# Performance work log

Hardware: AMD Instinct MI355X
Metric: run time of the kernel (lower is better)

## Reference

```python
import jax, jax.numpy as jnp
import numpy as np

G, N, F, H, E = 3, 40000, 256, 128, 640000


def gcn_conv(x, W, b, edge_index):
    """PyG GCNConv: x @ W, add self-loops, sym-normalized scatter-add, + bias."""
    n = x.shape[0]
    x = x @ W
    loop = jnp.arange(n)
    row = jnp.concatenate([edge_index[0], loop])  # source nodes
    col = jnp.concatenate([edge_index[1], loop])  # target nodes
    deg = jax.ops.segment_sum(jnp.ones_like(row, dtype=x.dtype), col, num_segments=n)
    dinv = jnp.where(deg > 0, jax.lax.rsqrt(jnp.maximum(deg, 1e-12)), 0.0)
    norm = dinv[row] * dinv[col]
    out = jax.ops.segment_sum(x[row] * norm[:, None], col, num_segments=n)
    return out + b


def setup_inputs() -> dict:
    key = jax.random.key(0)
    ks = jax.random.split(key, 14)
    inp = {
        'x': jax.random.normal(ks[0], (G, N, F), jnp.float32),
        'edge_index': jax.random.randint(ks[1], (G, 2, E), 0, N, jnp.int64),
        'fc1_W': jax.random.normal(ks[2], (G, F, H), jnp.float32) * 0.05,
        'fc1_b': jax.random.normal(ks[3], (G, H), jnp.float32) * 0.05,
        'conv1_W': jax.random.normal(ks[4], (G, H, H), jnp.float32) * 0.05,
        'conv1_b': jax.random.normal(ks[5], (G, H), jnp.float32) * 0.05,
        'conv2_W': jax.random.normal(ks[6], (G, H, H), jnp.float32) * 0.05,
        'conv2_b': jax.random.normal(ks[7], (G, H), jnp.float32) * 0.05,
        'dconv1_W': jax.random.normal(ks[8], (G, H, H), jnp.float32) * 0.05,
        'dconv1_b': jax.random.normal(ks[9], (G, H), jnp.float32) * 0.05,
        'dconv2_W': jax.random.normal(ks[10], (G, H, H), jnp.float32) * 0.05,
        'dconv2_b': jax.random.normal(ks[11], (G, H), jnp.float32) * 0.05,
        'fc2_W': jax.random.normal(ks[12], (H, F), jnp.float32) * 0.05,
        'fc2_b': jax.random.normal(ks[13], (F,), jnp.float32) * 0.05,
    }
    return inp


def reference(x, edge_index, fc1_W, fc1_b, conv1_W, conv1_b, conv2_W, conv2_b,
              dconv1_W, dconv1_b, dconv2_W, dconv2_b, fc2_W, fc2_b):
    def encoder(xi, ei, fw, fb, c1w, c1b, c2w, c2b):
        pre = xi @ fw + fb                     # fc1
        h = gcn_conv(pre, c1w, c1b, ei)
        h = gcn_conv(h, c2w, c2b, ei)
        return pre, jax.nn.relu(h)

    pre_feat, enc = jax.vmap(encoder)(x, edge_index, fc1_W, fc1_b,
                                      conv1_W, conv1_b, conv2_W, conv2_b)

    # Faithful reproduction of the sequentially-mutating cross-graph block.
    h = [enc[i] for i in range(G)]
    for i in range(G):
        for j in range(G):
            if j != i:
                h[i] = h[i] + h[j]
        h[i] = h[G - 1] - h[i]  # loop var j ends at G-1 (zeroes tensor when i==G-1)
        h[i] = gcn_conv(h[i], dconv1_W[i], dconv1_b[i], edge_index[i])
        h[i] = gcn_conv(h[i], dconv2_W[i], dconv2_b[i], edge_index[i])

    fin_feat = h[0]
    for k in range(1, G - 1):
        fin_feat = fin_feat + h[k]

    loss_embedding = jax.nn.softmax(fin_feat @ fc2_W + fc2_b, axis=-1)
    return pre_feat, enc, jnp.stack(h), fin_feat, loss_embedding
```

## Files before the change

kernel.cpp:

```cpp
#include <hip/hip_runtime.h>
#include <hip/hip_bf16.h>

#define NV 40000
#define FD 256
#define HD 128
#define ED 640000
#define NG 3
#define NH (NV*HD)

#define CH  64
#define EPC (ED/CH)
#define NB  625

typedef unsigned short u16;
typedef unsigned int   u32;
typedef __attribute__((ext_vector_type(8))) u16    u16x8;
typedef __attribute__((ext_vector_type(8))) __bf16 bf16x8;
typedef __attribute__((ext_vector_type(4))) float  f32x4;

__device__ inline u16 f2b(float f){ __bf16 h = (__bf16)f; return __builtin_bit_cast(u16, h); }
__device__ inline float b2f(u16 u){ u32 x = ((u32)u)<<16; return __builtin_bit_cast(float, x); }

__global__ __launch_bounds__(256) void histB_k(const int* __restrict__ ei, int* __restrict__ btot){
  int ch=blockIdx.x, g=blockIdx.y, t=threadIdx.x;
  __shared__ int h[NB];
  for (int i=t;i<NB;i+=256) h[i]=0;
  __syncthreads();
  const int* cc = ei + (long)g*2*ED + ED + ch*EPC;
  for (int j=t;j<EPC;j+=256) atomicAdd(&h[cc[j]>>6],1);
  __syncthreads();
  for (int b=t;b<NB;b+=256){ int v=h[b]; if(v) atomicAdd(&btot[g*NB+b], v); }
}

__global__ void scanB_k(const int* __restrict__ btot, int* __restrict__ base, int* __restrict__ gcur){
  __shared__ int wsum[16];
  int tid=threadIdx.x, lane=tid&63, wv=tid>>6;
  for (int g=0; g<NG; ++g){
    int v = (tid<NB)? btot[g*NB+tid] : 0;
    int s=v;
    #pragma unroll
    for (int d=1; d<64; d<<=1){ int u=__shfl_up(s,d,64); if(lane>=d) s+=u; }
    if (lane==63) wsum[wv]=s;
    __syncthreads();
    if (wv==0){
      int t3=(lane<16)?wsum[lane]:0;
      #pragma unroll
      for (int d=1; d<16; d<<=1){ int u=__shfl_up(t3,d,64); if(lane>=d) t3+=u; }
      if (lane<16) wsum[lane]=t3;
    }
    __syncthreads();
    int incl = s + (wv>0? wsum[wv-1]:0);
    if (tid<NB){
      base[g*(NB+1)+tid]=incl-v;
      gcur[g*NB+tid]=incl-v;
      if (tid==NB-1) base[g*(NB+1)+NB]=incl;
    }
    __syncthreads();
  }
}

__global__ __launch_bounds__(256) void scat_k(const int* __restrict__ ei, int* __restrict__ gcur,
                                              u32* __restrict__ temp){
  int ch=blockIdx.x, g=blockIdx.y, t=threadIdx.x;
  __shared__ int h[NB];
  __shared__ int cur[NB];
  for (int i=t;i<NB;i+=256) h[i]=0;
  __syncthreads();
  const int* rr = ei + (long)g*2*ED + ch*EPC;
  const int* cc = rr + ED;
  for (int j=t;j<EPC;j+=256) atomicAdd(&h[cc[j]>>6],1);
  __syncthreads();
  for (int b=t;b<NB;b+=256){ int v=h[b]; cur[b] = v? atomicAdd(&gcur[g*NB+b], v) : 0; }
  __syncthreads();
  u32* tg = temp + (long)g*ED;
  for (int j=t;j<EPC;j+=256){
    int r=rr[j], c=cc[j];
    int pos=atomicAdd(&cur[c>>6],1);
    tg[pos]=((u32)(c&63)<<16)|(u32)r;
  }
}

__global__ __launch_bounds__(256) void sort_k(const u32* __restrict__ temp, const int* __restrict__ base,
                                              u16* __restrict__ csr, int* __restrict__ cptr,
                                              float* __restrict__ dinv){
  int b=blockIdx.x, g=blockIdx.y, t=threadIdx.x;
  __shared__ int cnt[64];
  __shared__ int cur[64];
  if (t<64) cnt[t]=0;
  __syncthreads();
  const u32* tg = temp + (long)g*ED;
  int s=base[g*(NB+1)+b], e=base[g*(NB+1)+b+1];
  for (int i=s+t;i<e;i+=256) atomicAdd(&cnt[tg[i]>>16],1);
  __syncthreads();
  if (t<64){
    int v=cnt[t];
    int sc=v;
    #pragma unroll
    for (int d=1;d<64;d<<=1){ int u=__shfl_up(sc,d,64); if(t>=d) sc+=u; }
    int st = s + sc - v;
    cur[t]=st;
    cptr[(long)g*(NV+1) + b*64 + t] = st;
    if (b==NB-1 && t==63) cptr[(long)g*(NV+1)+NV] = e;
    dinv[(long)g*NV + b*64 + t] = rsqrtf((float)v+1.0f);
  }
  __syncthreads();
  u16* cg = csr + (long)g*ED;
  for (int i=s+t;i<e;i+=256){
    u32 tt=tg[i];
    int pos=atomicAdd(&cur[tt>>16],1);
    cg[pos]=(u16)(tt&0xFFFF);
  }
}

__global__ __launch_bounds__(256) void svec_k(const u16* __restrict__ csr, const int* __restrict__ cptr,
                                              const float* __restrict__ dinv, float* __restrict__ sv,
                                              int totWaves){
  int wid=(int)((blockIdx.x*256+threadIdx.x)>>6);
  if (wid>=totWaves) return;
  int lane=threadIdx.x&63;
  int g=wid/NV, c=wid-g*NV;
  const u16* cg=csr+(long)g*ED;
  const int* cp=cptr+(long)g*(NV+1);
  const float* dv=dinv+(long)g*NV;
  int j0=cp[c], j1=cp[c+1];
  float sum=0.f;
  for (int j=j0+lane;j<j1;j+=64) sum+=dv[cg[j]];
  #pragma unroll
  for (int o=32;o;o>>=1) sum+=__shfl_xor(sum,o,64);
  if (lane==0){ float dc=dv[c]; sv[(long)g*NV+c]=dc*(dc+sum); }
}

__device__ inline void tr_seg(const float* __restrict__ src, u16* __restrict__ dst,
                              int K, int NN, long idx, long total){
  if (idx>=total) return;
  long per=(long)K*NN; long mat=idx/per; long rem=idx-mat*per;
  int k=(int)(rem/NN), c=(int)(rem-(long)k*NN);
  dst[mat*per+(long)c*K+k]=f2b(src[idx]);
}

__global__ __launch_bounds__(256) void trall_k(
    const float* fc1W, const float* fc2W,
    const float* c1W, const float* c2W, const float* c1b,
    const float* d1W, const float* d2W, const float* d1b,
    u16* w_fc1, u16* w_fc2, u16* w_ce, u16* w_cd,
    float* t_enc, float* t_dec)
{
  int blk=blockIdx.x, t=threadIdx.x;
  if (blk < 384){
    tr_seg(fc1W, w_fc1, FD, HD, (long)blk*256+t, (long)NG*FD*HD);
  } else if (blk < 512){
    tr_seg(fc2W, w_fc2, HD, FD, (long)(blk-384)*256+t, (long)HD*FD);
  } else if (blk < 832){
    int bb=blk-512;
    int mat=bb>>6;
    int local=(bb&63)*256+t;
    int n=local>>7, k=local&127;
    const float* W1; const float* W2; u16* dst;
    if (mat<3){ W1=c1W+(long)mat*HD*HD; W2=c2W+(long)mat*HD*HD; dst=w_ce+(long)mat*HD*HD; }
    else { int md=mat-3; W1=d1W+(long)md*HD*HD; W2=d2W+(long)md*HD*HD; dst=w_cd+(long)md*HD*HD; }
    float s=0.f;
    for (int j=0;j<HD;j++) s += W1[k*HD+j]*W2[j*HD+n];
    dst[(long)n*HD+k]=f2b(s);
  } else {
    for (int idx=t; idx<768; idx+=256){
      int which=idx>>7, n=idx&127;
      const float* b; const float* W; float* dst;
      if (which<3){ b=c1b+which*HD; W=c2W+(long)which*HD*HD; dst=t_enc+which*HD; }
      else { int w2=which-3; b=d1b+w2*HD; W=d2W+(long)w2*HD*HD; dst=t_dec+w2*HD; }
      float s=0.f;
      for (int k=0;k<HD;k++) s += b[k]*W[(long)k*HD+n];
      dst[n]=s;
    }
  }
}

template<int MODE, int EX>
__global__ __launch_bounds__(256) void gemm_k(
    const void* __restrict__ A_, long sA,
    const u16* __restrict__ Bt, long sB,
    const float* __restrict__ biasCol, long sBias,
    const float* __restrict__ svec, long sS,
    const float* __restrict__ tvec,
    const float* __restrict__ scaleRow, long sSc,
    const float* __restrict__ Add,
    float* __restrict__ Cf, long sCf,
    float* __restrict__ Cf2,
    u16* __restrict__ Cb, long sCb,
    int M, int N, int K, int relu)
{
  __shared__ __align__(16) u16 lsA[128*64];
  __shared__ __align__(16) u16 lsB[128*64];
  const int gz = blockIdx.z;
  const float* Af = (const float*)A_ + (long)gz*sA;
  const u16*   Ab = (const u16*)  A_ + (long)gz*sA;
  const u16* Bp = Bt + (long)gz*sB;
  const int t = threadIdx.x;
  const int lane = t & 63, wv = t >> 6, wm = wv >> 1, wn = wv & 1;
  const int lr = lane & 15, lq = lane >> 4;
  const int ar = t >> 1, ah = t & 1;
  const long grow = (long)blockIdx.x*128 + ar;
  const int colB = blockIdx.y*128 + ar;

  f32x4 acc[4][4];
  #pragma unroll
  for (int m=0;m<4;m++)
    #pragma unroll
    for (int n=0;n<4;n++) acc[m][n] = (f32x4)(0.0f);

  for (int k0=0; k0<K; k0+=64){
    if (k0) __syncthreads();
    u16x8 av[4];
    if (grow < M){
      if (MODE==0){
        const u16x8* s = (const u16x8*)(Ab + grow*(long)K + k0 + ah*32);
        #pragma unroll
        for (int i=0;i<4;i++) av[i] = s[i];
      } else {
        const float4* s = (const float4*)(Af + grow*(long)K + k0 + ah*32);
        #pragma unroll
        for (int i=0;i<4;i++){
          float4 v0 = s[i*2], v1 = s[i*2+1];
          u16x8 w;
          w[0]=f2b(v0.x); w[1]=f2b(v0.y); w[2]=f2b(v0.z); w[3]=f2b(v0.w);
          w[4]=f2b(v1.x); w[5]=f2b(v1.y); w[6]=f2b(v1.z); w[7]=f2b(v1.w);
          av[i] = w;
        }
      }
    } else {
      #pragma unroll
      for (int i=0;i<4;i++) av[i] = (u16x8)((u16)0);
    }
    #pragma unroll
    for (int i=0;i<4;i++){
      int q = ah*4 + i;
      *(u16x8*)&lsA[ar*64 + ((q ^ (ar&7))<<3)] = av[i];
    }
    {
      const u16x8* s = (const u16x8*)(Bp + (long)colB*K + k0 + ah*32);
      #pragma unroll
      for (int i=0;i<4;i++){
        int q = ah*4 + i;
        *(u16x8*)&lsB[ar*64 + ((q ^ (ar&7))<<3)] = s[i];
      }
    }
    __syncthreads();
    #pragma unroll
    for (int kk=0; kk<2; kk++){
      bf16x8 afr[4], bfr[4];
      #pragma unroll
      for (int m=0;m<4;m++){
        int r = wm*64 + m*16 + lr;
        int q = kk*4 + lq;
        afr[m] = __builtin_bit_cast(bf16x8, *(const u16x8*)&lsA[r*64 + ((q ^ (r&7))<<3)]);
      }
      #pragma unroll
      for (int n=0;n<4;n++){
        int r = wn*64 + n*16 + lr;
        int q = kk*4 + lq;
        bfr[n] = __builtin_bit_cast(bf16x8, *(const u16x8*)&lsB[r*64 + ((q ^ (r&7))<<3)]);
      }
      #pragma unroll
      for (int m=0;m<4;m++)
        #pragma unroll
        for (int n=0;n<4;n++)
          acc[m][n] = __builtin_amdgcn_mfma_f32_16x16x32_bf16(afr[m], bfr[n], acc[m][n], 0, 0, 0);
    }
  }
  #pragma unroll
  for (int m=0;m<4;m++){
    long gr0 = (long)blockIdx.x*128 + wm*64 + m*16 + lq*4;
    #pragma unroll
    for (int n=0;n<4;n++){
      int gc = blockIdx.y*128 + wn*64 + n*16 + lr;
      float bb = biasCol[gz*sBias + gc];
      float tv = (svec!=nullptr) ? tvec[gz*sBias + gc] : 0.0f;
      #pragma unroll
      for (int i=0;i<4;i++){
        long gr = gr0 + i;
        if (gr < M){
          float v = acc[m][n][i] + bb;
          if (svec!=nullptr) v += svec[gz*sS + gr]*tv;
          if (relu) v = fmaxf(v, 0.0f);
          if (EX==0){
            if (Cf) Cf[gz*sCf + gr*(long)N + gc] = v;
            if (Cb){
              float sc = scaleRow ? scaleRow[gz*sSc + gr] : 1.0f;
              Cb[gz*sCb + gr*(long)N + gc] = f2b(v*sc);
            }
          } else if (EX==1){
            Cf[gz*sCf + gr*(long)N + gc] = v;
            float z = -(v + Add[gr*(long)N + gc]) * scaleRow[gr];
            Cb[gz*sCb + gr*(long)N + gc] = f2b(z);
          } else {
            Cf[gz*sCf + gr*(long)N + gc] = v;
            Cf2[gr*(long)N + gc] = v + Add[gr*(long)N + gc];
          }
        }
      }
    }
  }
}

__global__ __launch_bounds__(256) void agg_k(
    const u16* __restrict__ xw, long sXW,
    const u16* __restrict__ csr, long sCsr,
    const int* __restrict__ cptr, long sCp,
    const float* __restrict__ dinv, long sD,
    u16* __restrict__ outB, long sOB,
    int totWaves, int scOut)
{
  int wid = (int)((blockIdx.x*256 + threadIdx.x) >> 6);
  if (wid >= totWaves) return;
  int lane = threadIdx.x & 63;
  int g = wid / NV;
  int c = wid - g*NV;
  const u32* xp = (const u32*)(xw + (long)g*sXW);
  const u16* cg = csr + (long)g*sCsr;
  const int* cp = cptr + (long)g*sCp;
  float dc = dinv[(long)g*sD + c];
  u32 u = xp[(long)c*64 + lane];
  float sx = b2f((u16)u), sy = b2f((u16)(u>>16));
  int j0 = cp[c], j1 = cp[c+1];
  int deg = j1 - j0;
  int idx = 0;
  if (lane < deg) idx = cg[j0 + lane];
  int kmax = min(deg, 64);
  int k = 0;
  for (; k+4<=kmax; k+=4){
    int r0=__shfl(idx,k,64), r1=__shfl(idx,k+1,64), r2=__shfl(idx,k+2,64), r3=__shfl(idx,k+3,64);
    u32 v0=xp[(long)r0*64+lane], v1=xp[(long)r1*64+lane];
    u32 v2=xp[(long)r2*64+lane], v3=xp[(long)r3*64+lane];
    sx += b2f((u16)v0); sy += b2f((u16)(v0>>16));
    sx += b2f((u16)v1); sy += b2f((u16)(v1>>16));
    sx += b2f((u16)v2); sy += b2f((u16)(v2>>16));
    sx += b2f((u16)v3); sy += b2f((u16)(v3>>16));
  }
  for (; k<kmax; ++k){
    int r=__shfl(idx,k,64);
    u32 v=xp[(long)r*64+lane];
    sx += b2f((u16)v); sy += b2f((u16)(v>>16));
  }
  for (int j=j0+64; j<j1; ++j){
    int r=cg[j];
    u32 v=xp[(long)r*64+lane];
    sx += b2f((u16)v); sy += b2f((u16)(v>>16));
  }
  float m = scOut ? dc*dc : dc;
  float ox = m*sx, oy = m*sy;
  ((u32*)(outB + (long)g*sOB))[(long)c*64 + lane] = (u32)f2b(ox) | ((u32)f2b(oy)<<16);
}

__global__ void ewz_k(const float4* __restrict__ e0, const float4* __restrict__ e1,
                      const float* __restrict__ dinv0, u16* __restrict__ outB){
  int i = blockIdx.x*256 + threadIdx.x;
  if (i >= NH/4) return;
  int row = i>>5;
  float d = dinv0[row];
  float4 a = e0[i], b = e1[i];
  float x0=-d*(a.x+b.x), x1=-d*(a.y+b.y), x2=-d*(a.z+b.z), x3=-d*(a.w+b.w);
  ((uint2*)outB)[i] = make_uint2((u32)f2b(x0) | ((u32)f2b(x1)<<16),
                                 (u32)f2b(x2) | ((u32)f2b(x3)<<16));
}

__global__ void h2_k(const float* __restrict__ sv2, const float* __restrict__ t2,
                     const float* __restrict__ b2, float4* __restrict__ outF){
  int i = blockIdx.x*256 + threadIdx.x;
  if (i >= NH/4) return;
  int row = i>>5, c4 = i&31;
  float s = sv2[row];
  float4 tv = ((const float4*)t2)[c4];
  float4 bb = ((const float4*)b2)[c4];
  outF[i] = make_float4(s*tv.x+bb.x, s*tv.y+bb.y, s*tv.z+bb.z, s*tv.w+bb.w);
}

__global__ void softmax_k(float* __restrict__ d, int rows){
  int wid = (blockIdx.x*256 + threadIdx.x) >> 6;
  if (wid >= rows) return;
  int lane = threadIdx.x & 63;
  float4* p = (float4*)(d + (long)wid*FD);
  float4 v = p[lane];
  float m = fmaxf(fmaxf(v.x, v.y), fmaxf(v.z, v.w));
  #pragma unroll
  for (int o=32; o; o>>=1) m = fmaxf(m, __shfl_xor(m, o, 64));
  float e0 = __expf(v.x-m), e1 = __expf(v.y-m), e2 = __expf(v.z-m), e3 = __expf(v.w-m);
  float s = e0+e1+e2+e3;
  #pragma unroll
  for (int o=32; o; o>>=1) s += __shfl_xor(s, o, 64);
  float inv = 1.0f/s;
  p[lane] = make_float4(e0*inv, e1*inv, e2*inv, e3*inv);
}

extern "C" void kernel_launch(void* const* d_in, const int* in_sizes, int n_in,
                              void* d_out, int out_size, void* d_ws, size_t ws_size,
                              hipStream_t stream)
{
  const float* x    = (const float*)d_in[0];
  const int*   ei   = (const int*)  d_in[1];
  const float* fc1W = (const float*)d_in[2];
  const float* fc1b = (const float*)d_in[3];
  const float* c1W  = (const float*)d_in[4];
  const float* c1b  = (const float*)d_in[5];
  const float* c2W  = (const float*)d_in[6];
  const float* c2b  = (const float*)d_in[7];
  const float* d1W  = (const float*)d_in[8];
  const float* d1b  = (const float*)d_in[9];
  const float* d2W  = (const float*)d_in[10];
  const float* d2b  = (const float*)d_in[11];
  const float* fc2W = (const float*)d_in[12];
  const float* fc2b = (const float*)d_in[13];
  (void)in_sizes; (void)n_in; (void)out_size; (void)ws_size;

  float* out  = (float*)d_out;
  float* O_pre = out;
  float* O_enc = out + (long)NG*NH;
  float* O_h   = out + 2L*NG*NH;
  float* O_fin = out + 3L*NG*NH;
  float* O_ls  = O_fin + NH;

  char* p = (char*)d_ws;
  auto alloc = [&](size_t bytes)->void*{
    void* r = (void*)p; p += (bytes + 255) & ~(size_t)255; return r;
  };
  u16* bfA    = (u16*)alloc((size_t)NG*NH*2);
  u16* bfB    = (u16*)alloc((size_t)NG*NH*2);
  u16* bfC    = (u16*)alloc((size_t)NG*NH*2);
  u16* wt_fc1 = (u16*)alloc((size_t)NG*FD*HD*2);
  u16* wt_fc2 = (u16*)alloc((size_t)HD*FD*2);
  u16* wt_ce  = (u16*)alloc((size_t)NG*HD*HD*2);
  u16* wt_cd  = (u16*)alloc((size_t)2*HD*HD*2);
  float* t_enc = (float*)alloc((size_t)NG*HD*4);
  float* t_dec = (float*)alloc((size_t)NG*HD*4);
  u32*  temp  = (u32*) alloc((size_t)NG*ED*4);
  u16*  csr   = (u16*) alloc((size_t)NG*ED*2);
  int*  cptr  = (int*) alloc((size_t)NG*(NV+1)*4);
  int*  btot  = (int*) alloc((size_t)NG*NB*4);
  int*  base  = (int*) alloc((size_t)NG*(NB+1)*4);
  int*  gcur  = (int*) alloc((size_t)NG*NB*4);
  float* dinv = (float*)alloc((size_t)NG*NV*4);
  float* svec = (float*)alloc((size_t)NG*NV*4);

  hipMemsetAsync(btot, 0, (size_t)NG*NB*4, stream);
  histB_k<<<dim3(CH,NG), 256, 0, stream>>>(ei, btot);
  scanB_k<<<1, 1024, 0, stream>>>(btot, base, gcur);
  scat_k<<<dim3(CH,NG), 256, 0, stream>>>(ei, gcur, temp);
  sort_k<<<dim3(NB,NG), 256, 0, stream>>>(temp, base, csr, cptr, dinv);
  svec_k<<<NG*NV/4, 256, 0, stream>>>(csr, cptr, dinv, svec, NG*NV);

  trall_k<<<833, 256, 0, stream>>>(fc1W, fc2W, c1W, c2W, c1b, d1W, d2W, d1b,
                                   wt_fc1, wt_fc2, wt_ce, wt_cd, t_enc, t_dec);

  dim3 g3((NV+127)/128, 1, NG);
  dim3 g1((NV+127)/128, 1, 1);
  dim3 gf((NV+127)/128, 2, 1);

  gemm_k<1,0><<<g3, 256, 0, stream>>>(x, (long)NV*FD, wt_fc1, (long)FD*HD, fc1b, HD,
                                      nullptr, 0, nullptr, dinv, NV, nullptr,
                                      O_pre, NH, nullptr, bfA, NH, NV, HD, FD, 0);
  agg_k<<<NG*NV/4, 256, 0, stream>>>(bfA, NH, csr, ED, cptr, NV+1, dinv, NV, bfB, NH, NG*NV, 1);
  agg_k<<<NG*NV/4, 256, 0, stream>>>(bfB, NH, csr, ED, cptr, NV+1, dinv, NV, bfC, NH, NG*NV, 0);
  gemm_k<0,0><<<g3, 256, 0, stream>>>(bfC, NH, wt_ce, (long)HD*HD, c2b, HD,
                                      svec, NV, t_enc, nullptr, 0, nullptr,
                                      O_enc, NH, nullptr, nullptr, 0, NV, HD, HD, 1);

  h2_k<<<NH/4/256, 256, 0, stream>>>(svec + 2L*NV, t_dec + 2*HD, d2b + 2*HD, (float4*)(O_h + 2L*NH));

  ewz_k<<<NH/4/256, 256, 0, stream>>>((const float4*)O_enc, (const float4*)(O_enc+NH), dinv, bfA);
  agg_k<<<NV/4, 256, 0, stream>>>(bfA, 0, csr, 0, cptr, 0, dinv, 0, bfB, 0, NV, 1);
  agg_k<<<NV/4, 256, 0, stream>>>(bfB, 0, csr, 0, cptr, 0, dinv, 0, bfC, 0, NV, 0);
  gemm_k<0,1><<<g1, 256, 0, stream>>>(bfC, 0, wt_cd, 0, d2b, 0,
                                      svec, 0, t_dec, dinv + NV, 0, O_enc + NH,
                                      O_h, 0, nullptr, bfA, 0, NV, HD, HD, 0);

  agg_k<<<NV/4, 256, 0, stream>>>(bfA, 0, csr + (long)ED, 0, cptr + (NV+1), 0, dinv + NV, 0, bfB, 0, NV, 1);
  agg_k<<<NV/4, 256, 0, stream>>>(bfB, 0, csr + (long)ED, 0, cptr + (NV+1), 0, dinv + NV, 0, bfC, 0, NV, 0);
  gemm_k<0,2><<<g1, 256, 0, stream>>>(bfC, 0, wt_cd + (long)HD*HD, 0, d2b + HD, 0,
                                      svec + NV, 0, t_dec + HD, nullptr, 0, O_h,
                                      O_h + NH, 0, O_fin, nullptr, 0, NV, HD, HD, 0);

  gemm_k<1,0><<<gf, 256, 0, stream>>>(O_fin, 0, wt_fc2, 0, fc2b, 0,
                                      nullptr, 0, nullptr, nullptr, 0, nullptr,
                                      O_ls, 0, nullptr, nullptr, 0, NV, FD, HD, 0);
  softmax_k<<<NV/4, 256, 0, stream>>>(O_ls, NV);
}
```

Measured before the change: 603.7 us.

## Fuse fc2 GEMM with softmax, merge elementwise kernels, widen aggregation unroll

```diff
diff --git a/kernel.cpp b/kernel.cpp
--- a/kernel.cpp
+++ b/kernel.cpp
@@ -293,7 +293,9 @@
             Cb[gz*sCb + gr*(long)N + gc] = f2b(z);
           } else {
             Cf[gz*sCf + gr*(long)N + gc] = v;
-            Cf2[gr*(long)N + gc] = v + Add[gr*(long)N + gc];
+            float fv = v + Add[gr*(long)N + gc];
+            Cf2[gr*(long)N + gc] = fv;
+            if (Cb) Cb[gz*sCb + gr*(long)N + gc] = f2b(fv);
           }
         }
       }
@@ -318,7 +320,7 @@
   const u16* cg = csr + (long)g*sCsr;
   const int* cp = cptr + (long)g*sCp;
   float dc = dinv[(long)g*sD + c];
-  u32 u = xp[(long)c*64 + lane];
+  u32 u = xp[(c<<6) + lane];
   float sx = b2f((u16)u), sy = b2f((u16)(u>>16));
   int j0 = cp[c], j1 = cp[c+1];
   int deg = j1 - j0;
@@ -326,68 +328,196 @@
   if (lane < deg) idx = cg[j0 + lane];
   int kmax = min(deg, 64);
   int k = 0;
-  for (; k+4<=kmax; k+=4){
-    int r0=__shfl(idx,k,64), r1=__shfl(idx,k+1,64), r2=__shfl(idx,k+2,64), r3=__shfl(idx,k+3,64);
-    u32 v0=xp[(long)r0*64+lane], v1=xp[(long)r1*64+lane];
-    u32 v2=xp[(long)r2*64+lane], v3=xp[(long)r3*64+lane];
+  for (; k+8<=kmax; k+=8){
+    int r0=__shfl(idx,k,64),   r1=__shfl(idx,k+1,64), r2=__shfl(idx,k+2,64), r3=__shfl(idx,k+3,64);
+    int r4=__shfl(idx,k+4,64), r5=__shfl(idx,k+5,64), r6=__shfl(idx,k+6,64), r7=__shfl(idx,k+7,64);
+    u32 v0=xp[(r0<<6)+lane], v1=xp[(r1<<6)+lane], v2=xp[(r2<<6)+lane], v3=xp[(r3<<6)+lane];
+    u32 v4=xp[(r4<<6)+lane], v5=xp[(r5<<6)+lane], v6=xp[(r6<<6)+lane], v7=xp[(r7<<6)+lane];
     sx += b2f((u16)v0); sy += b2f((u16)(v0>>16));
     sx += b2f((u16)v1); sy += b2f((u16)(v1>>16));
     sx += b2f((u16)v2); sy += b2f((u16)(v2>>16));
     sx += b2f((u16)v3); sy += b2f((u16)(v3>>16));
+    sx += b2f((u16)v4); sy += b2f((u16)(v4>>16));
+    sx += b2f((u16)v5); sy += b2f((u16)(v5>>16));
+    sx += b2f((u16)v6); sy += b2f((u16)(v6>>16));
+    sx += b2f((u16)v7); sy += b2f((u16)(v7>>16));
+  }
+  for (; k+4<=kmax; k+=4){
+    int r0=__shfl(idx,k,64), r1=__shfl(idx,k+1,64), r2=__shfl(idx,k+2,64), r3=__shfl(idx,k+3,64);
+    u32 v0=xp[(r0<<6)+lane], v1=xp[(r1<<6)+lane], v2=xp[(r2<<6)+lane], v3=xp[(r3<<6)+lane];
+    sx += b2f((u16)v0); sy += b2f((u16)(v0>>16));
+    sx += b2f((u16)v1); sy += b2f((u16)(v1>>16));
+    sx += b2f((u16)v2); sy += b2f((u16)(v2>>16));
+    sx += b2f((u16)v3); sy += b2f((u16)(v3>>16));
   }
   for (; k<kmax; ++k){
     int r=__shfl(idx,k,64);
-    u32 v=xp[(long)r*64+lane];
+    u32 v=xp[(r<<6)+lane];
     sx += b2f((u16)v); sy += b2f((u16)(v>>16));
   }
   for (int j=j0+64; j<j1; ++j){
     int r=cg[j];
-    u32 v=xp[(long)r*64+lane];
+    u32 v=xp[(r<<6)+lane];
     sx += b2f((u16)v); sy += b2f((u16)(v>>16));
   }
   float m = scOut ? dc*dc : dc;
   float ox = m*sx, oy = m*sy;
-  ((u32*)(outB + (long)g*sOB))[(long)c*64 + lane] = (u32)f2b(ox) | ((u32)f2b(oy)<<16);
-}
-
-__global__ void ewz_k(const float4* __restrict__ e0, const float4* __restrict__ e1,
-                      const float* __restrict__ dinv0, u16* __restrict__ outB){
-  int i = blockIdx.x*256 + threadIdx.x;
-  if (i >= NH/4) return;
-  int row = i>>5;
-  float d = dinv0[row];
-  float4 a = e0[i], b = e1[i];
-  float x0=-d*(a.x+b.x), x1=-d*(a.y+b.y), x2=-d*(a.z+b.z), x3=-d*(a.w+b.w);
-  ((uint2*)outB)[i] = make_uint2((u32)f2b(x0) | ((u32)f2b(x1)<<16),
-                                 (u32)f2b(x2) | ((u32)f2b(x3)<<16));
-}
-
-__global__ void h2_k(const float* __restrict__ sv2, const float* __restrict__ t2,
-                     const float* __restrict__ b2, float4* __restrict__ outF){
-  int i = blockIdx.x*256 + threadIdx.x;
-  if (i >= NH/4) return;
-  int row = i>>5, c4 = i&31;
-  float s = sv2[row];
-  float4 tv = ((const float4*)t2)[c4];
-  float4 bb = ((const float4*)b2)[c4];
-  outF[i] = make_float4(s*tv.x+bb.x, s*tv.y+bb.y, s*tv.z+bb.z, s*tv.w+bb.w);
-}
-
-__global__ void softmax_k(float* __restrict__ d, int rows){
-  int wid = (blockIdx.x*256 + threadIdx.x) >> 6;
-  if (wid >= rows) return;
-  int lane = threadIdx.x & 63;
-  float4* p = (float4*)(d + (long)wid*FD);
-  float4 v = p[lane];
-  float m = fmaxf(fmaxf(v.x, v.y), fmaxf(v.z, v.w));
-  #pragma unroll
-  for (int o=32; o; o>>=1) m = fmaxf(m, __shfl_xor(m, o, 64));
-  float e0 = __expf(v.x-m), e1 = __expf(v.y-m), e2 = __expf(v.z-m), e3 = __expf(v.w-m);
-  float s = e0+e1+e2+e3;
-  #pragma unroll
-  for (int o=32; o; o>>=1) s += __shfl_xor(s, o, 64);
-  float inv = 1.0f/s;
-  p[lane] = make_float4(e0*inv, e1*inv, e2*inv, e3*inv);
+  ((u32*)(outB + (long)g*sOB))[(c<<6) + lane] = (u32)f2b(ox) | ((u32)f2b(oy)<<16);
+}
+
+__global__ void ewzh2_k(const float4* __restrict__ e0, const float4* __restrict__ e1,
+                        const float* __restrict__ dinv0, u16* __restrict__ outB,
+                        const float* __restrict__ sv2, const float* __restrict__ t2,
+                        const float* __restrict__ b2, float4* __restrict__ outH2){
+  int blk = blockIdx.x;
+  if (blk < (NH/4)/256){
+    int i = blk*256 + threadIdx.x;
+    int row = i>>5;
+    float d = dinv0[row];
+    float4 a = e0[i], b = e1[i];
+    float x0=-d*(a.x+b.x), x1=-d*(a.y+b.y), x2=-d*(a.z+b.z), x3=-d*(a.w+b.w);
+    ((uint2*)outB)[i] = make_uint2((u32)f2b(x0) | ((u32)f2b(x1)<<16),
+                                   (u32)f2b(x2) | ((u32)f2b(x3)<<16));
+  } else {
+    int i = (blk - (NH/4)/256)*256 + threadIdx.x;
+    int row = i>>5, c4 = i&31;
+    float s = sv2[row];
+    float4 tv = ((const float4*)t2)[c4];
+    float4 bb = ((const float4*)b2)[c4];
+    outH2[i] = make_float4(s*tv.x+bb.x, s*tv.y+bb.y, s*tv.z+bb.z, s*tv.w+bb.w);
+  }
+}
+
+__global__ __launch_bounds__(256) void fc2sm_k(
+    const u16* __restrict__ Ab, const u16* __restrict__ Bw,
+    const float* __restrict__ bias, float* __restrict__ Out, int M)
+{
+  __shared__ __align__(16) u16 lsA[128*64];
+  __shared__ __align__(16) u16 lsB[256*64];
+  const int t = threadIdx.x;
+  const int lane = t & 63, wv = t >> 6, wm = wv >> 1, wn = wv & 1;
+  const int lr = lane & 15, lq = lane >> 4;
+  const int ar = t >> 1, ah = t & 1;
+  const long grow = (long)blockIdx.x*128 + ar;
+
+  f32x4 acc[4][8];
+  #pragma unroll
+  for (int m=0;m<4;m++)
+    #pragma unroll
+    for (int n=0;n<8;n++) acc[m][n] = (f32x4)(0.0f);
+
+  for (int k0=0; k0<128; k0+=64){
+    if (k0) __syncthreads();
+    {
+      u16x8 av[4];
+      if (grow < M){
+        const u16x8* s = (const u16x8*)(Ab + grow*128L + k0 + ah*32);
+        #pragma unroll
+        for (int i=0;i<4;i++) av[i] = s[i];
+      } else {
+        #pragma unroll
+        for (int i=0;i<4;i++) av[i] = (u16x8)((u16)0);
+      }
+      #pragma unroll
+      for (int i=0;i<4;i++){
+        int q = ah*4 + i;
+        *(u16x8*)&lsA[ar*64 + ((q ^ (ar&7))<<3)] = av[i];
+      }
+    }
+    #pragma unroll
+    for (int rr=0; rr<2; rr++){
+      int r = ar + rr*128;
+      const u16x8* s = (const u16x8*)(Bw + (long)r*128 + k0 + ah*32);
+      #pragma unroll
+      for (int i=0;i<4;i++){
+        int q = ah*4 + i;
+        *(u16x8*)&lsB[r*64 + ((q ^ (r&7))<<3)] = s[i];
+      }
+    }
+    __syncthreads();
+    #pragma unroll
+    for (int kk=0; kk<2; kk++){
+      bf16x8 afr[4], bfr[8];
+      #pragma unroll
+      for (int m=0;m<4;m++){
+        int r = wm*64 + m*16 + lr;
+        int q = kk*4 + lq;
+        afr[m] = __builtin_bit_cast(bf16x8, *(const u16x8*)&lsA[r*64 + ((q ^ (r&7))<<3)]);
+      }
+      #pragma unroll
+      for (int n=0;n<8;n++){
+        int r = wn*128 + n*16 + lr;
+        int q = kk*4 + lq;
+        bfr[n] = __builtin_bit_cast(bf16x8, *(const u16x8*)&lsB[r*64 + ((q ^ (r&7))<<3)]);
+      }
+      #pragma unroll
+      for (int m=0;m<4;m++)
+        #pragma unroll
+        for (int n=0;n<8;n++)
+          acc[m][n] = __builtin_amdgcn_mfma_f32_16x16x32_bf16(afr[m], bfr[n], acc[m][n], 0, 0, 0);
+    }
+  }
+  #pragma unroll
+  for (int n=0;n<8;n++){
+    float bb = bias[wn*128 + n*16 + lr];
+    #pragma unroll
+    for (int m=0;m<4;m++)
+      #pragma unroll
+      for (int i=0;i<4;i++) acc[m][n][i] += bb;
+  }
+  __syncthreads();
+  float* lsF = (float*)lsA;
+  float pmax[4][4];
+  #pragma unroll
+  for (int m=0;m<4;m++)
+    #pragma unroll
+    for (int i=0;i<4;i++){
+      float v = acc[m][0][i];
+      #pragma unroll
+      for (int n=1;n<8;n++) v = fmaxf(v, acc[m][n][i]);
+      #pragma unroll
+      for (int o=8;o;o>>=1) v = fmaxf(v, __shfl_xor(v, o, 16));
+      pmax[m][i] = v;
+      if (lr==0) lsF[(wm*64 + m*16 + lq*4 + i)*2 + wn] = v;
+    }
+  __syncthreads();
+  float psum[4][4];
+  #pragma unroll
+  for (int m=0;m<4;m++)
+    #pragma unroll
+    for (int i=0;i<4;i++){
+      int rl = wm*64 + m*16 + lq*4 + i;
+      float rm = fmaxf(lsF[rl*2], lsF[rl*2+1]);
+      float s = 0.f;
+      #pragma unroll
+      for (int n=0;n<8;n++){
+        float e = __expf(acc[m][n][i] - rm);
+        acc[m][n][i] = e;
+        s += e;
+      }
+      #pragma unroll
+      for (int o=8;o;o>>=1) s += __shfl_xor(s, o, 16);
+      psum[m][i] = s;
+      if (lr==0) lsF[256 + rl*2 + wn] = s;
+    }
+  __syncthreads();
+  #pragma unroll
+  for (int m=0;m<4;m++){
+    long gr0 = (long)blockIdx.x*128 + wm*64 + m*16 + lq*4;
+    #pragma unroll
+    for (int i=0;i<4;i++){
+      long gr = gr0 + i;
+      if (gr < M){
+        int rl = wm*64 + m*16 + lq*4 + i;
+        float inv = 1.0f/(lsF[256 + rl*2] + lsF[256 + rl*2 + 1]);
+        #pragma unroll
+        for (int n=0;n<8;n++){
+          int gc = wn*128 + n*16 + lr;
+          Out[gr*256L + gc] = acc[m][n][i]*inv;
+        }
+      }
+    }
+  }
 }
 
 extern "C" void kernel_launch(void* const* d_in, const int* in_sizes, int n_in,
@@ -451,7 +581,6 @@
 
   dim3 g3((NV+127)/128, 1, NG);
   dim3 g1((NV+127)/128, 1, 1);
-  dim3 gf((NV+127)/128, 2, 1);
 
   gemm_k<1,0><<<g3, 256, 0, stream>>>(x, (long)NV*FD, wt_fc1, (long)FD*HD, fc1b, HD,
                                       nullptr, 0, nullptr, dinv, NV, nullptr,
@@ -462,9 +591,10 @@
                                       svec, NV, t_enc, nullptr, 0, nullptr,
                                       O_enc, NH, nullptr, nullptr, 0, NV, HD, HD, 1);
 
-  h2_k<<<NH/4/256, 256, 0, stream>>>(svec + 2L*NV, t_dec + 2*HD, d2b + 2*HD, (float4*)(O_h + 2L*NH));
-
-  ewz_k<<<NH/4/256, 256, 0, stream>>>((const float4*)O_enc, (const float4*)(O_enc+NH), dinv, bfA);
+  ewzh2_k<<<2*(NH/4)/256, 256, 0, stream>>>((const float4*)O_enc, (const float4*)(O_enc+NH), dinv, bfA,
+                                            svec + 2L*NV, t_dec + 2*HD, d2b + 2*HD,
+                                            (float4*)(O_h + 2L*NH));
+
   agg_k<<<NV/4, 256, 0, stream>>>(bfA, 0, csr, 0, cptr, 0, dinv, 0, bfB, 0, NV, 1);
   agg_k<<<NV/4, 256, 0, stream>>>(bfB, 0, csr, 0, cptr, 0, dinv, 0, bfC, 0, NV, 0);
   gemm_k<0,1><<<g1, 256, 0, stream>>>(bfC, 0, wt_cd, 0, d2b, 0,
@@ -475,10 +605,7 @@
   agg_k<<<NV/4, 256, 0, stream>>>(bfB, 0, csr + (long)ED, 0, cptr + (NV+1), 0, dinv + NV, 0, bfC, 0, NV, 0);
   gemm_k<0,2><<<g1, 256, 0, stream>>>(bfC, 0, wt_cd + (long)HD*HD, 0, d2b + HD, 0,
                                       svec + NV, 0, t_dec + HD, nullptr, 0, O_h,
-                                      O_h + NH, 0, O_fin, nullptr, 0, NV, HD, HD, 0);
-
-  gemm_k<1,0><<<gf, 256, 0, stream>>>(O_fin, 0, wt_fc2, 0, fc2b, 0,
-                                      nullptr, 0, nullptr, nullptr, 0, nullptr,
-                                      O_ls, 0, nullptr, nullptr, 0, NV, FD, HD, 0);
-  softmax_k<<<NV/4, 256, 0, stream>>>(O_ls, NV);
-}
+                                      O_h + NH, 0, O_fin, bfA, 0, NV, HD, HD, 0);
+
+  fc2sm_k<<<(NV+127)/128, 256, 0, stream>>>(bfA, wt_fc2, fc2b, O_ls, NV);
+}
```

New measurement: 592.4 us. No clear change (-1.9%).
